# Performance work log

Measured on AMD Instinct MI355X. Metric: run time of the kernel, lower is better.

Reference implementation:

```python
import jax, jax.numpy as jnp
import numpy as np

N = 50000   # nodes
E = 600000  # edges
D = 128     # emb_dim
L = 5       # num_layers
ATOM_DIMS = np.array([119, 4, 11, 13, 11, 7, 13, 2, 9]) + 5   # per-feature vocab (+5 as in source)
BOND_DIMS = np.array([7, 22, 2]) + 5
BL_CENTERS = np.arange(0.0, 2.0, 0.1, dtype=np.float32)   # 20 centers, gamma 10
PR_CENTERS = np.arange(0.0, 1.0, 0.05, dtype=np.float32)  # 20 centers, gamma 1
BL_GAMMA = 10.0
PR_GAMMA = 1.0
BN_EPS = 1e-5


def setup_inputs() -> dict:
    key = jax.random.key(0)
    ks = jax.random.split(key, 16)
    scale = 1.0 / np.sqrt(D)
    atom_off = jnp.asarray(np.concatenate([[0], np.cumsum(ATOM_DIMS)[:-1]]), jnp.int32)
    bond_off = jnp.asarray(np.concatenate([[0], np.cumsum(BOND_DIMS)[:-1]]), jnp.int32)
    return {
        "x": jax.random.randint(ks[0], (N, 9), 0, 7, dtype=jnp.int32),
        "edge_index": jax.random.randint(ks[1], (2, E), 0, N, dtype=jnp.int32),
        "edge_attr_int": jax.random.randint(ks[2], (E, 3), 0, 7, dtype=jnp.int32),
        "edge_attr_float": jax.random.uniform(ks[3], (E, 2), dtype=jnp.float32),
        "atom_off": atom_off,
        "bond_off": bond_off,
        "atom_emb": jax.random.normal(ks[4], (int(ATOM_DIMS.sum()), D), jnp.float32) * scale,
        "bond_emb": jax.random.normal(ks[5], (L, int(BOND_DIMS.sum()), D), jnp.float32) * scale,
        "W_bl": jax.random.normal(ks[6], (L, len(BL_CENTERS), D), jnp.float32) * scale,
        "b_bl": jnp.zeros((L, D), jnp.float32),
        "W_pr": jax.random.normal(ks[7], (L, len(PR_CENTERS), D), jnp.float32) * scale,
        "b_pr": jnp.zeros((L, D), jnp.float32),
        "mlp_W1": jax.random.normal(ks[8], (L, D, D), jnp.float32) * scale,
        "mlp_b1": jnp.zeros((L, D), jnp.float32),
        "bn1_g": jnp.ones((L, D), jnp.float32),
        "bn1_b": jnp.zeros((L, D), jnp.float32),
        "mlp_W2": jax.random.normal(ks[9], (L, D, D), jnp.float32) * scale,
        "mlp_b2": jnp.zeros((L, D), jnp.float32),
        "eps_gin": jnp.zeros((L,), jnp.float32),
        "bn_g": jnp.ones((L, D), jnp.float32),
        "bn_b": jnp.zeros((L, D), jnp.float32),
    }


def _bn(h, g, b):
    # BatchNorm1d, training-mode batch statistics over the node axis
    m = h.mean(0)
    v = h.var(0)
    return (h - m) * jax.lax.rsqrt(v + BN_EPS) * g + b


def _rbf(x, centers, gamma):
    # exp(-gamma * (x - c)^2): [E] -> [E, n_centers]
    return jnp.exp(-gamma * jnp.square(x[:, None] - centers[None, :]))


def reference(x, edge_index, edge_attr_int, edge_attr_float, atom_off, bond_off,
              atom_emb, bond_emb, W_bl, b_bl, W_pr, b_pr,
              mlp_W1, mlp_b1, bn1_g, bn1_b, mlp_W2, mlp_b2,
              eps_gin, bn_g, bn_b):
    # AtomEncoder: sum of 9 categorical embeddings (flat table + offsets)
    h = atom_emb[x + atom_off[None, :]].sum(1)  # [N, D]
    src, dst = edge_index[0], edge_index[1]
    bl = _rbf(edge_attr_float[:, 0], jnp.asarray(BL_CENTERS), BL_GAMMA)  # [E, 20]
    pr = _rbf(edge_attr_float[:, 1], jnp.asarray(PR_CENTERS), PR_GAMMA)  # [E, 20]
    for l in range(L):
        # per-layer edge embedding: BondEncoder + BondFloatRBF
        e = bond_emb[l][edge_attr_int + bond_off[None, :]].sum(1)
        e = e + bl @ W_bl[l] + b_bl[l] + pr @ W_pr[l] + b_pr[l]
        # GINConv (aggr='add'): mlp((1+eps)*x + sum_j relu(x_j + e_ij))
        msg = jax.nn.relu(h[src] + e)                       # [E, D]
        agg = jax.ops.segment_sum(msg, dst, num_segments=N)  # [N, D]
        z = (1.0 + eps_gin[l]) * h + agg
        z = z @ mlp_W1[l] + mlp_b1[l]
        z = jax.nn.relu(_bn(z, bn1_g[l], bn1_b[l]))
        z = z @ mlp_W2[l] + mlp_b2[l]
        # outer per-layer BatchNorm; ReLU except last layer (drop_ratio=0)
        z = _bn(z, bn_g[l], bn_b[l])
        if l < L - 1:
            z = jax.nn.relu(z)
        h = z
    return h  # JK='last'
```

## Files before the change

kernel.cpp:

```cpp
#include <hip/hip_runtime.h>
#include <hip/hip_bf16.h>

#define GN 50000
#define GE 600000
#define DD 128
#define TQ 4096
#define NBOND 2268
#define TROWS (2*(TQ+1) + NBOND)
#define SCB 49
#define NBANK 16
#define SSET (NBANK*256)
#define NB 782
#define LDA2 132

typedef __attribute__((ext_vector_type(8))) short short8;
typedef __attribute__((ext_vector_type(4))) float floatx4;

__device__ __forceinline__ unsigned short f2b(float f) {
    __hip_bfloat16 h = __float2bfloat16(f);
    return __builtin_bit_cast(unsigned short, h);
}
__device__ __forceinline__ float b2f_lo(unsigned int u) { return __uint_as_float(u << 16); }
__device__ __forceinline__ float b2f_hi(unsigned int u) { return __uint_as_float(u & 0xffff0000u); }
__device__ __forceinline__ float bs2f(short s) {
    return __uint_as_float(((unsigned int)(unsigned short)s) << 16);
}

__global__ __launch_bounds__(256) void atom_kernel(
    const int* __restrict__ x, const int* __restrict__ atom_off,
    const float* __restrict__ atom_emb, unsigned short* __restrict__ h)
{
    int t = blockIdx.x * 256 + threadIdx.x;
    if (t >= GN * DD) return;
    int n = t >> 7, d = t & 127;
    float s = 0.f;
#pragma unroll
    for (int f = 0; f < 9; f++) {
        int idx = x[n * 9 + f] + atom_off[f];
        s += atom_emb[idx * DD + d];
    }
    h[t] = f2b(s);
}

__global__ __launch_bounds__(256) void hist_kernel(const int* __restrict__ ei, int* __restrict__ count)
{
    int e = blockIdx.x * 256 + threadIdx.x;
    if (e < GE) atomicAdd(&count[ei[GE + e]], 1);
}

__global__ __launch_bounds__(1024) void scan1_kernel(
    const int* __restrict__ count, int* __restrict__ row_start, int* __restrict__ blocksum)
{
    __shared__ int sh[1024];
    int t = threadIdx.x;
    int idx = blockIdx.x * 1024 + t;
    int v = (idx < GN) ? count[idx] : 0;
    sh[t] = v;
    __syncthreads();
    for (int off = 1; off < 1024; off <<= 1) {
        int u = (t >= off) ? sh[t - off] : 0;
        __syncthreads();
        sh[t] += u;
        __syncthreads();
    }
    if (idx <= GN) row_start[idx] = (t == 0) ? 0 : sh[t - 1];
    if (t == 1023) blocksum[blockIdx.x] = sh[1023];
}

__global__ __launch_bounds__(64) void scan2_kernel(
    const int* __restrict__ blocksum, int* __restrict__ blockoff)
{
    int t = threadIdx.x;
    int v = (t < SCB) ? blocksum[t] : 0;
#pragma unroll
    for (int off = 1; off < 64; off <<= 1) {
        int u = __shfl_up(v, off);
        if (t >= off) v += u;
    }
    int e = __shfl_up(v, 1);
    if (t == 0) e = 0;
    if (t < SCB) blockoff[t] = e;
}

__global__ __launch_bounds__(1024) void scan3_kernel(
    int* __restrict__ row_start, const int* __restrict__ blockoff)
{
    int idx = blockIdx.x * 1024 + threadIdx.x;
    if (idx <= GN) row_start[idx] += blockoff[blockIdx.x];
}

__global__ __launch_bounds__(256) void scatter_kernel(
    const int* __restrict__ ei, const int* __restrict__ eai, const float* __restrict__ eaf,
    const int* __restrict__ row_start, int* __restrict__ fill, int4* __restrict__ ep)
{
    int e = blockIdx.x * 256 + threadIdx.x;
    if (e < GE) {
        int d = ei[GE + e];
        int p = row_start[d] + atomicAdd(&fill[d], 1);
        int src = ei[e];
        float x1 = eaf[2 * e], x2 = eaf[2 * e + 1];
        int q1 = (int)(x1 * (float)TQ + 0.5f); q1 = min(max(q1, 0), TQ);
        int q2 = (int)(x2 * (float)TQ + 0.5f); q2 = min(max(q2, 0), TQ);
        int b0 = eai[3 * e], b1 = eai[3 * e + 1], b2 = eai[3 * e + 2];
        ep[p] = make_int4(src, q1 | (q2 << 16), (b0 * 27 + b1) * 7 + b2, 0);
    }
}

__global__ __launch_bounds__(128) void tables_kernel(
    const float* __restrict__ W_bl, const float* __restrict__ b_bl,
    const float* __restrict__ W_pr, const float* __restrict__ b_pr,
    const float* __restrict__ bond_emb, const int* __restrict__ bond_off,
    unsigned short* __restrict__ tbl_bl, unsigned short* __restrict__ tbl_pr,
    unsigned short* __restrict__ tbl_bond)
{
    int l = blockIdx.x / TROWS;
    int b = blockIdx.x % TROWS;
    int d = threadIdx.x;
    const float* W_bl_l = W_bl + (size_t)l * 20 * DD;
    const float* W_pr_l = W_pr + (size_t)l * 20 * DD;
    const float* bemb_l = bond_emb + (size_t)l * 46 * DD;
    if (b < (TQ + 1)) {
        float xq = b * (1.0f / TQ);
        float s = b_bl[(size_t)l * DD + d] + b_pr[(size_t)l * DD + d];
#pragma unroll
        for (int k = 0; k < 20; k++) {
            float dl = xq - 0.1f * k;
            s += __expf(-10.f * dl * dl) * W_bl_l[k * DD + d];
        }
        tbl_bl[((size_t)l * (TQ + 1) + b) * DD + d] = f2b(s);
    } else if (b < 2 * (TQ + 1)) {
        int q = b - (TQ + 1);
        float xq = q * (1.0f / TQ);
        float s = 0.f;
#pragma unroll
        for (int k = 0; k < 20; k++) {
            float dl = xq - 0.05f * k;
            s += __expf(-dl * dl) * W_pr_l[k * DD + d];
        }
        tbl_pr[((size_t)l * (TQ + 1) + q) * DD + d] = f2b(s);
    } else {
        int r = b - 2 * (TQ + 1);
        int b0 = r / 189;
        int rem = r % 189;
        int b1 = rem / 7, b2 = rem % 7;
        tbl_bond[((size_t)l * NBOND + r) * DD + d] =
            f2b(bemb_l[(b0 + bond_off[0]) * DD + d]
              + bemb_l[(b1 + bond_off[1]) * DD + d]
              + bemb_l[(b2 + bond_off[2]) * DD + d]);
    }
}

__global__ __launch_bounds__(256) void wfrag_kernel(
    const float* __restrict__ W1, const float* __restrict__ W2,
    unsigned short* __restrict__ wf_hi, unsigned short* __restrict__ wf_lo)
{
    int t = blockIdx.x * 256 + threadIdx.x;
    if (t >= 10 * 2048) return;
    int mat = t >> 11;
    int rem = t & 2047;
    int kt = rem >> 9;
    int rem2 = rem & 511;
    int nt = rem2 >> 6;
    int lane = rem2 & 63;
    const float* src = (mat & 1) ? (W2 + (size_t)(mat >> 1) * DD * DD)
                                 : (W1 + (size_t)(mat >> 1) * DD * DD);
    int n = nt * 16 + (lane & 15);
    int k0 = kt * 32 + (lane >> 4) * 8;
    size_t base = (size_t)mat * 16384 + (size_t)((kt * 8 + nt) * 64 + lane) * 8;
#pragma unroll
    for (int j = 0; j < 8; j++) {
        float w = src[(size_t)(k0 + j) * DD + n];
        unsigned short hi = f2b(w);
        wf_hi[base + j] = hi;
        wf_lo[base + j] = f2b(w - bs2f((short)hi));
    }
}

__global__ __launch_bounds__(256) void edge_kernel(
    const int4* __restrict__ ep,
    const unsigned short* __restrict__ tbl_bl, const unsigned short* __restrict__ tbl_pr,
    const unsigned short* __restrict__ tbl_bond,
    const unsigned short* __restrict__ hsrc, const int* __restrict__ row_start,
    const float* __restrict__ eps_gin, int layer, int apply_bn,
    const float* __restrict__ stats_prev, const float* __restrict__ g_prev,
    const float* __restrict__ b_prev,
    float* __restrict__ A)
{
    __shared__ float sc_s[DD], tr_s[DD];
    int tid = threadIdx.x;
    if (tid < DD) {
        float sc = 1.f, tr = 0.f;
        if (apply_bn) {
            float s = 0.f, q = 0.f;
#pragma unroll
            for (int bk = 0; bk < NBANK; bk++) {
                s += stats_prev[bk * 256 + tid];
                q += stats_prev[bk * 256 + 128 + tid];
            }
            float m = s * (1.0f / GN);
            float v = q * (1.0f / GN) - m * m;
            sc = g_prev[tid] * rsqrtf(v + 1e-5f);
            tr = b_prev[tid] - m * sc;
        }
        sc_s[tid] = sc;
        tr_s[tid] = tr;
    }
    __syncthreads();

    int wid = __builtin_amdgcn_readfirstlane(tid >> 6);
    int lane = tid & 63;
    float sc0 = sc_s[2 * lane],     tr0 = tr_s[2 * lane];
    float sc1 = sc_s[2 * lane + 1], tr1 = tr_s[2 * lane + 1];
    float rmin = apply_bn ? 0.f : -__builtin_inff();

    int n = blockIdx.x * 4 + wid;
    int s0 = __builtin_amdgcn_readfirstlane(row_start[n]);
    int s1 = __builtin_amdgcn_readfirstlane(row_start[n + 1]);
    const unsigned int* hu = (const unsigned int*)hsrc;
    const unsigned int* tb = (const unsigned int*)tbl_bl;
    const unsigned int* tp = (const unsigned int*)tbl_pr;
    const unsigned int* tg = (const unsigned int*)tbl_bond;
    float a0 = 0.f, a1 = 0.f;
    int p = s0;
    for (; p + 2 <= s1; p += 2) {
        int4 m0 = ep[p];
        int4 m1 = ep[p + 1];
        unsigned int ub0 = tb[(size_t)(m0.y & 0xffff) * 64 + lane];
        unsigned int up0 = tp[(size_t)((unsigned)m0.y >> 16) * 64 + lane];
        unsigned int ug0 = tg[(size_t)m0.z * 64 + lane];
        unsigned int uh0 = hu[(size_t)m0.x * 64 + lane];
        unsigned int ub1 = tb[(size_t)(m1.y & 0xffff) * 64 + lane];
        unsigned int up1 = tp[(size_t)((unsigned)m1.y >> 16) * 64 + lane];
        unsigned int ug1 = tg[(size_t)m1.z * 64 + lane];
        unsigned int uh1 = hu[(size_t)m1.x * 64 + lane];
        float h00 = fmaxf(fmaf(b2f_lo(uh0), sc0, tr0), rmin);
        float h01 = fmaxf(fmaf(b2f_hi(uh0), sc1, tr1), rmin);
        float h10 = fmaxf(fmaf(b2f_lo(uh1), sc0, tr0), rmin);
        float h11 = fmaxf(fmaf(b2f_hi(uh1), sc1, tr1), rmin);
        a0 += fmaxf(h00 + b2f_lo(ub0) + b2f_lo(up0) + b2f_lo(ug0), 0.f);
        a1 += fmaxf(h01 + b2f_hi(ub0) + b2f_hi(up0) + b2f_hi(ug0), 0.f);
        a0 += fmaxf(h10 + b2f_lo(ub1) + b2f_lo(up1) + b2f_lo(ug1), 0.f);
        a1 += fmaxf(h11 + b2f_hi(ub1) + b2f_hi(up1) + b2f_hi(ug1), 0.f);
    }
    if (p < s1) {
        int4 m0 = ep[p];
        unsigned int ub0 = tb[(size_t)(m0.y & 0xffff) * 64 + lane];
        unsigned int up0 = tp[(size_t)((unsigned)m0.y >> 16) * 64 + lane];
        unsigned int ug0 = tg[(size_t)m0.z * 64 + lane];
        unsigned int uh0 = hu[(size_t)m0.x * 64 + lane];
        float h00 = fmaxf(fmaf(b2f_lo(uh0), sc0, tr0), rmin);
        float h01 = fmaxf(fmaf(b2f_hi(uh0), sc1, tr1), rmin);
        a0 += fmaxf(h00 + b2f_lo(ub0) + b2f_lo(up0) + b2f_lo(ug0), 0.f);
        a1 += fmaxf(h01 + b2f_hi(ub0) + b2f_hi(up0) + b2f_hi(ug0), 0.f);
    }
    float eps1 = 1.f + eps_gin[layer];
    unsigned int un = hu[(size_t)n * 64 + lane];
    a0 += eps1 * fmaxf(fmaf(b2f_lo(un), sc0, tr0), rmin);
    a1 += eps1 * fmaxf(fmaf(b2f_hi(un), sc1, tr1), rmin);
    float2 o; o.x = a0; o.y = a1;
    *(float2*)(A + (size_t)n * DD + 2 * lane) = o;
}

template <int MODE>
__global__ __launch_bounds__(256) void gemm_kernel(
    const float* __restrict__ Asrc,
    const unsigned short* __restrict__ wf_hi, const unsigned short* __restrict__ wf_lo,
    const float* __restrict__ bias,
    unsigned short* __restrict__ Cbf, float* __restrict__ Cf32, int out_bf16,
    const float* __restrict__ stats_in, const float* __restrict__ bn_g,
    const float* __restrict__ bn_b, float* __restrict__ stats_out)
{
    __shared__ float At[64 * LDA2];
    __shared__ float sc_s[DD], tr_s[DD];
    int tid = threadIdx.x, wid = tid >> 6, lane = tid & 63;
    int row0 = blockIdx.x * 64;

    if (MODE == 1) {
        if (tid < DD) {
            float s = 0.f, q = 0.f;
#pragma unroll
            for (int bk = 0; bk < NBANK; bk++) {
                s += stats_in[bk * 256 + tid];
                q += stats_in[bk * 256 + 128 + tid];
            }
            float m = s * (1.0f / GN);
            float v = q * (1.0f / GN) - m * m;
            float sc = bn_g[tid] * rsqrtf(v + 1e-5f);
            sc_s[tid] = sc;
            tr_s[tid] = bn_b[tid] - m * sc;
        }
    }

    {
        const float* g = Asrc + (size_t)row0 * DD;
#pragma unroll
        for (int i = 0; i < 8; i++) {
            int idx = i * 1024 + tid * 4;
            float4 v = *(const float4*)(g + idx);
            int r = idx >> 7, c = idx & 127;
            *(float4*)(At + r * LDA2 + c) = v;
        }
    }
    __syncthreads();

    int quad = lane >> 4, l16 = lane & 15;
    floatx4 acc[4][2];
#pragma unroll
    for (int rt = 0; rt < 4; rt++)
#pragma unroll
        for (int nt = 0; nt < 2; nt++) acc[rt][nt] = (floatx4){0.f, 0.f, 0.f, 0.f};

    const short8* bhp = (const short8*)wf_hi;
    const short8* blp = (const short8*)wf_lo;
#pragma unroll
    for (int kt = 0; kt < 4; kt++) {
        short8 ahi[4], alo[4];
        int kb = kt * 32 + quad * 8;
#pragma unroll
        for (int rt = 0; rt < 4; rt++) {
            const float* ap = At + (rt * 16 + l16) * LDA2 + kb;
            float a[8];
            *(float4*)(a)     = *(const float4*)(ap);
            *(float4*)(a + 4) = *(const float4*)(ap + 4);
            if (MODE == 1) {
#pragma unroll
                for (int j = 0; j < 8; j++)
                    a[j] = fmaxf(a[j] * sc_s[kb + j] + tr_s[kb + j], 0.f);
            }
#pragma unroll
            for (int j = 0; j < 8; j++) {
                unsigned short hi = f2b(a[j]);
                ahi[rt][j] = (short)hi;
                alo[rt][j] = (short)f2b(a[j] - bs2f((short)hi));
            }
        }
#pragma unroll
        for (int nt = 0; nt < 2; nt++) {
            int ntg = wid * 2 + nt;
            short8 bhi = bhp[(kt * 8 + ntg) * 64 + lane];
            short8 blo = blp[(kt * 8 + ntg) * 64 + lane];
#pragma unroll
            for (int rt = 0; rt < 4; rt++) {
                acc[rt][nt] = __builtin_amdgcn_mfma_f32_16x16x32_bf16(ahi[rt], bhi, acc[rt][nt], 0, 0, 0);
                acc[rt][nt] = __builtin_amdgcn_mfma_f32_16x16x32_bf16(alo[rt], bhi, acc[rt][nt], 0, 0, 0);
                acc[rt][nt] = __builtin_amdgcn_mfma_f32_16x16x32_bf16(ahi[rt], blo, acc[rt][nt], 0, 0, 0);
            }
        }
    }

    int bank = blockIdx.x & (NBANK - 1);
#pragma unroll
    for (int nt = 0; nt < 2; nt++) {
        int col = (wid * 2 + nt) * 16 + l16;
        float bv = bias[col];
        float s = 0.f, q = 0.f;
#pragma unroll
        for (int rt = 0; rt < 4; rt++) {
#pragma unroll
            for (int v = 0; v < 4; v++) {
                int r = row0 + rt * 16 + quad * 4 + v;
                float o = acc[rt][nt][v] + bv;
                if (r < GN) {
                    s += o; q += o * o;
                    if (MODE == 1 && out_bf16) Cbf[(size_t)r * DD + col] = f2b(o);
                    else                       Cf32[(size_t)r * DD + col] = o;
                }
            }
        }
        s += __shfl_xor(s, 16); s += __shfl_xor(s, 32);
        q += __shfl_xor(q, 16); q += __shfl_xor(q, 32);
        if (lane < 16) {
            atomicAdd(&stats_out[bank * 256 + col], s);
            atomicAdd(&stats_out[bank * 256 + 128 + col], q);
        }
    }
}

__global__ __launch_bounds__(256) void bn_apply_kernel(
    const float* __restrict__ Z, const float* __restrict__ stats2,
    const float* __restrict__ g, const float* __restrict__ b,
    float* __restrict__ fout)
{
    __shared__ float sc_s[DD], tr_s[DD];
    int tid = threadIdx.x;
    if (tid < DD) {
        float s = 0.f, q = 0.f;
#pragma unroll
        for (int bk = 0; bk < NBANK; bk++) {
            s += stats2[bk * 256 + tid];
            q += stats2[bk * 256 + 128 + tid];
        }
        float m = s * (1.0f / GN);
        float v = q * (1.0f / GN) - m * m;
        float sc = g[tid] * rsqrtf(v + 1e-5f);
        sc_s[tid] = sc;
        tr_s[tid] = b[tid] - m * sc;
    }
    __syncthreads();
    const int total = GN * DD;
    for (int t = blockIdx.x * 256 + tid; t < total; t += gridDim.x * 256) {
        int c = t & 127;
        fout[t] = Z[t] * sc_s[c] + tr_s[c];
    }
}

extern "C" void kernel_launch(void* const* d_in, const int* in_sizes, int n_in,
                              void* d_out, int out_size, void* d_ws, size_t ws_size,
                              hipStream_t stream)
{
    const int*   x        = (const int*)d_in[0];
    const int*   ei       = (const int*)d_in[1];
    const int*   eai      = (const int*)d_in[2];
    const float* eaf      = (const float*)d_in[3];
    const int*   atom_off = (const int*)d_in[4];
    const int*   bond_off = (const int*)d_in[5];
    const float* atom_emb = (const float*)d_in[6];
    const float* bond_emb = (const float*)d_in[7];
    const float* W_bl     = (const float*)d_in[8];
    const float* b_bl     = (const float*)d_in[9];
    const float* W_pr     = (const float*)d_in[10];
    const float* b_pr     = (const float*)d_in[11];
    const float* W1       = (const float*)d_in[12];
    const float* b1       = (const float*)d_in[13];
    const float* bn1g     = (const float*)d_in[14];
    const float* bn1b     = (const float*)d_in[15];
    const float* W2       = (const float*)d_in[16];
    const float* b2       = (const float*)d_in[17];
    const float* eps_gin  = (const float*)d_in[18];
    const float* bng      = (const float*)d_in[19];
    const float* bnb      = (const float*)d_in[20];
    float* out = (float*)d_out;

    char* p = (char*)d_ws;
    unsigned short* h_bf  = (unsigned short*)p;  p += (size_t)GN * DD * 2;
    unsigned short* z2_bf = (unsigned short*)p;  p += (size_t)GN * DD * 2;
    float* A              = (float*)p;           p += (size_t)GN * DD * 4;
    float* z1             = (float*)p;           p += (size_t)GN * DD * 4;
    float* z2f            = (float*)p;           p += (size_t)GN * DD * 4;
    unsigned short* tbl_bl   = (unsigned short*)p;  p += (size_t)5 * (TQ + 1) * DD * 2;
    unsigned short* tbl_pr   = (unsigned short*)p;  p += (size_t)5 * (TQ + 1) * DD * 2;
    unsigned short* tbl_bond = (unsigned short*)p;  p += (size_t)5 * NBOND * DD * 2;
    unsigned short* wf_hi    = (unsigned short*)p;  p += (size_t)10 * 16384 * 2;
    unsigned short* wf_lo    = (unsigned short*)p;  p += (size_t)10 * 16384 * 2;
    float* stats_all = (float*)p;  p += (size_t)10 * SSET * 4;
    int* count    = (int*)p;    p += (size_t)GN * 4;
    int* fill     = (int*)p;    p += (size_t)GN * 4;
    int* row_start= (int*)p;    p += (size_t)(GN + 1) * 4;
    int* blocksum = (int*)p;    p += (size_t)SCB * 4;
    int* blockoff = (int*)p;    p += (size_t)SCB * 4;
    p = (char*)(((size_t)p + 15) & ~(size_t)15);
    int4* ep      = (int4*)p;   p += (size_t)GE * 16;

    hipMemsetAsync(count, 0, (size_t)GN * 4, stream);
    hipMemsetAsync(fill,  0, (size_t)GN * 4, stream);
    hipMemsetAsync(stats_all, 0, (size_t)10 * SSET * 4, stream);

    hist_kernel<<<(GE + 255) / 256, 256, 0, stream>>>(ei, count);
    scan1_kernel<<<SCB, 1024, 0, stream>>>(count, row_start, blocksum);
    scan2_kernel<<<1, 64, 0, stream>>>(blocksum, blockoff);
    scan3_kernel<<<SCB, 1024, 0, stream>>>(row_start, blockoff);
    scatter_kernel<<<(GE + 255) / 256, 256, 0, stream>>>(ei, eai, eaf, row_start, fill, ep);
    atom_kernel<<<(GN * DD + 255) / 256, 256, 0, stream>>>(x, atom_off, atom_emb, h_bf);
    wfrag_kernel<<<80, 256, 0, stream>>>(W1, W2, wf_hi, wf_lo);
    tables_kernel<<<5 * TROWS, 128, 0, stream>>>(
        W_bl, b_bl, W_pr, b_pr, bond_emb, bond_off, tbl_bl, tbl_pr, tbl_bond);

    for (int l = 0; l < 5; l++) {
        float* stats1 = stats_all + (size_t)(2 * l + 0) * SSET;
        float* stats2 = stats_all + (size_t)(2 * l + 1) * SSET;
        float* stats2_prev = stats_all + (size_t)(2 * (l - 1) + 1) * SSET;

        edge_kernel<<<GN / 4, 256, 0, stream>>>(
            ep,
            tbl_bl + (size_t)l * (TQ + 1) * DD,
            tbl_pr + (size_t)l * (TQ + 1) * DD,
            tbl_bond + (size_t)l * NBOND * DD,
            (l == 0) ? h_bf : z2_bf, row_start, eps_gin, l,
            (l > 0) ? 1 : 0,
            (l > 0) ? stats2_prev : stats_all,
            bng + (size_t)(l > 0 ? l - 1 : 0) * DD,
            bnb + (size_t)(l > 0 ? l - 1 : 0) * DD,
            A);

        gemm_kernel<0><<<NB, 256, 0, stream>>>(
            A, wf_hi + (size_t)(l * 2 + 0) * 16384, wf_lo + (size_t)(l * 2 + 0) * 16384,
            b1 + (size_t)l * DD, nullptr, z1, 0,
            nullptr, nullptr, nullptr, stats1);

        gemm_kernel<1><<<NB, 256, 0, stream>>>(
            z1, wf_hi + (size_t)(l * 2 + 1) * 16384, wf_lo + (size_t)(l * 2 + 1) * 16384,
            b2 + (size_t)l * DD, z2_bf, z2f, (l < 4) ? 1 : 0,
            stats1, bn1g + (size_t)l * DD, bn1b + (size_t)l * DD, stats2);
    }

    bn_apply_kernel<<<1024, 256, 0, stream>>>(
        z2f, stats_all + (size_t)9 * SSET, bng + (size_t)4 * DD, bnb + (size_t)4 * DD, out);
}
```

Before: 688.1 us.

## Switch edge aggregation to edge-parallel segmented atomics with separate BN prep pass

The per-destination-node edge kernel, where one wavefront walks a variable-length CSR row, is replaced by an edge-parallel kernel. Each wavefront takes 64 dst-sorted edges, accumulates runs that share a destination and flushes them with float atomics into A. A new hprep kernel applies the previous layer's BatchNorm and ReLU once per node, writes a bf16 copy of h, and initialises A with (1+eps)*h. Src and bond code are packed into one int so the dst can be stored, which assumes node index and bond code each fit in 16 bits. The change is meant to fix load imbalance and remove repeated BN math per edge, at the cost of an extra pass over the nodes, atomic traffic, and a now non-deterministic summation order.

```diff
diff --git a/kernel.cpp b/kernel.cpp
--- a/kernel.cpp
+++ b/kernel.cpp
@@ -12,6 +12,7 @@
 #define SSET (NBANK*256)
 #define NB 782
 #define LDA2 132
+#define EW (GE/64)
 
 typedef __attribute__((ext_vector_type(8))) short short8;
 typedef __attribute__((ext_vector_type(4))) float floatx4;
@@ -102,7 +103,8 @@
         int q1 = (int)(x1 * (float)TQ + 0.5f); q1 = min(max(q1, 0), TQ);
         int q2 = (int)(x2 * (float)TQ + 0.5f); q2 = min(max(q2, 0), TQ);
         int b0 = eai[3 * e], b1 = eai[3 * e + 1], b2 = eai[3 * e + 2];
-        ep[p] = make_int4(src, q1 | (q2 << 16), (b0 * 27 + b1) * 7 + b2, 0);
+        int bc = (b0 * 27 + b1) * 7 + b2;
+        ep[p] = make_int4(src | (bc << 16), q1 | (q2 << 16), d, 0);
     }
 }
 
@@ -176,89 +178,99 @@
     }
 }
 
+template <int L0>
+__global__ __launch_bounds__(256) void hprep_kernel(
+    const unsigned short* __restrict__ h_bf, const float* __restrict__ z2f,
+    const float* __restrict__ stats_prev, const float* __restrict__ g_prev,
+    const float* __restrict__ b_prev, const float* __restrict__ eps_gin, int layer,
+    unsigned short* __restrict__ hb, float* __restrict__ A)
+{
+    __shared__ float sc_s[DD], tr_s[DD];
+    int tid = threadIdx.x;
+    if (!L0) {
+        if (tid < DD) {
+            float s = 0.f, q = 0.f;
+#pragma unroll
+            for (int bk = 0; bk < NBANK; bk++) {
+                s += stats_prev[bk * 256 + tid];
+                q += stats_prev[bk * 256 + 128 + tid];
+            }
+            float m = s * (1.0f / GN);
+            float v = q * (1.0f / GN) - m * m;
+            float sc = g_prev[tid] * rsqrtf(v + 1e-5f);
+            sc_s[tid] = sc;
+            tr_s[tid] = b_prev[tid] - m * sc;
+        }
+        __syncthreads();
+    }
+    float eps1 = 1.f + eps_gin[layer];
+    const int total = GN * 64;
+    for (int t = blockIdx.x * 256 + tid; t < total; t += gridDim.x * 256) {
+        int d0 = (t & 63) * 2;
+        float f0, f1;
+        if (L0) {
+            unsigned int u = ((const unsigned int*)h_bf)[t];
+            f0 = b2f_lo(u); f1 = b2f_hi(u);
+        } else {
+            float2 z = ((const float2*)z2f)[t];
+            f0 = fmaxf(z.x * sc_s[d0] + tr_s[d0], 0.f);
+            f1 = fmaxf(z.y * sc_s[d0 + 1] + tr_s[d0 + 1], 0.f);
+            ((unsigned int*)hb)[t] = ((unsigned int)f2b(f1) << 16) | f2b(f0);
+        }
+        float2 o; o.x = eps1 * f0; o.y = eps1 * f1;
+        ((float2*)A)[t] = o;
+    }
+}
+
 __global__ __launch_bounds__(256) void edge_kernel(
     const int4* __restrict__ ep,
     const unsigned short* __restrict__ tbl_bl, const unsigned short* __restrict__ tbl_pr,
     const unsigned short* __restrict__ tbl_bond,
-    const unsigned short* __restrict__ hsrc, const int* __restrict__ row_start,
-    const float* __restrict__ eps_gin, int layer, int apply_bn,
-    const float* __restrict__ stats_prev, const float* __restrict__ g_prev,
-    const float* __restrict__ b_prev,
+    const unsigned short* __restrict__ hb,
     float* __restrict__ A)
 {
-    __shared__ float sc_s[DD], tr_s[DD];
     int tid = threadIdx.x;
-    if (tid < DD) {
-        float sc = 1.f, tr = 0.f;
-        if (apply_bn) {
-            float s = 0.f, q = 0.f;
-#pragma unroll
-            for (int bk = 0; bk < NBANK; bk++) {
-                s += stats_prev[bk * 256 + tid];
-                q += stats_prev[bk * 256 + 128 + tid];
-            }
-            float m = s * (1.0f / GN);
-            float v = q * (1.0f / GN) - m * m;
-            sc = g_prev[tid] * rsqrtf(v + 1e-5f);
-            tr = b_prev[tid] - m * sc;
-        }
-        sc_s[tid] = sc;
-        tr_s[tid] = tr;
-    }
-    __syncthreads();
-
-    int wid = __builtin_amdgcn_readfirstlane(tid >> 6);
+    int gw = blockIdx.x * 4 + (tid >> 6);
+    if (gw >= EW) return;
     int lane = tid & 63;
-    float sc0 = sc_s[2 * lane],     tr0 = tr_s[2 * lane];
-    float sc1 = sc_s[2 * lane + 1], tr1 = tr_s[2 * lane + 1];
-    float rmin = apply_bn ? 0.f : -__builtin_inff();
-
-    int n = blockIdx.x * 4 + wid;
-    int s0 = __builtin_amdgcn_readfirstlane(row_start[n]);
-    int s1 = __builtin_amdgcn_readfirstlane(row_start[n + 1]);
-    const unsigned int* hu = (const unsigned int*)hsrc;
+
+    int4 mv = ep[(size_t)gw * 64 + lane];
+
+    const unsigned int* hu = (const unsigned int*)hb;
     const unsigned int* tb = (const unsigned int*)tbl_bl;
     const unsigned int* tp = (const unsigned int*)tbl_pr;
     const unsigned int* tg = (const unsigned int*)tbl_bond;
+
     float a0 = 0.f, a1 = 0.f;
-    int p = s0;
-    for (; p + 2 <= s1; p += 2) {
-        int4 m0 = ep[p];
-        int4 m1 = ep[p + 1];
-        unsigned int ub0 = tb[(size_t)(m0.y & 0xffff) * 64 + lane];
-        unsigned int up0 = tp[(size_t)((unsigned)m0.y >> 16) * 64 + lane];
-        unsigned int ug0 = tg[(size_t)m0.z * 64 + lane];
-        unsigned int uh0 = hu[(size_t)m0.x * 64 + lane];
-        unsigned int ub1 = tb[(size_t)(m1.y & 0xffff) * 64 + lane];
-        unsigned int up1 = tp[(size_t)((unsigned)m1.y >> 16) * 64 + lane];
-        unsigned int ug1 = tg[(size_t)m1.z * 64 + lane];
-        unsigned int uh1 = hu[(size_t)m1.x * 64 + lane];
-        float h00 = fmaxf(fmaf(b2f_lo(uh0), sc0, tr0), rmin);
-        float h01 = fmaxf(fmaf(b2f_hi(uh0), sc1, tr1), rmin);
-        float h10 = fmaxf(fmaf(b2f_lo(uh1), sc0, tr0), rmin);
-        float h11 = fmaxf(fmaf(b2f_hi(uh1), sc1, tr1), rmin);
-        a0 += fmaxf(h00 + b2f_lo(ub0) + b2f_lo(up0) + b2f_lo(ug0), 0.f);
-        a1 += fmaxf(h01 + b2f_hi(ub0) + b2f_hi(up0) + b2f_hi(ug0), 0.f);
-        a0 += fmaxf(h10 + b2f_lo(ub1) + b2f_lo(up1) + b2f_lo(ug1), 0.f);
-        a1 += fmaxf(h11 + b2f_hi(ub1) + b2f_hi(up1) + b2f_hi(ug1), 0.f);
-    }
-    if (p < s1) {
-        int4 m0 = ep[p];
-        unsigned int ub0 = tb[(size_t)(m0.y & 0xffff) * 64 + lane];
-        unsigned int up0 = tp[(size_t)((unsigned)m0.y >> 16) * 64 + lane];
-        unsigned int ug0 = tg[(size_t)m0.z * 64 + lane];
-        unsigned int uh0 = hu[(size_t)m0.x * 64 + lane];
-        float h00 = fmaxf(fmaf(b2f_lo(uh0), sc0, tr0), rmin);
-        float h01 = fmaxf(fmaf(b2f_hi(uh0), sc1, tr1), rmin);
-        a0 += fmaxf(h00 + b2f_lo(ub0) + b2f_lo(up0) + b2f_lo(ug0), 0.f);
-        a1 += fmaxf(h01 + b2f_hi(ub0) + b2f_hi(up0) + b2f_hi(ug0), 0.f);
-    }
-    float eps1 = 1.f + eps_gin[layer];
-    unsigned int un = hu[(size_t)n * 64 + lane];
-    a0 += eps1 * fmaxf(fmaf(b2f_lo(un), sc0, tr0), rmin);
-    a1 += eps1 * fmaxf(fmaf(b2f_hi(un), sc1, tr1), rmin);
-    float2 o; o.x = a0; o.y = a1;
-    *(float2*)(A + (size_t)n * DD + 2 * lane) = o;
+    int cur = __builtin_amdgcn_readlane(mv.z, 0);
+
+    for (int b = 0; b < 8; b++) {
+        unsigned int ub[8], up[8], ug[8], uh[8];
+#pragma unroll
+        for (int u = 0; u < 8; u++) {
+            int j = b * 8 + u;
+            unsigned int sx = (unsigned int)__builtin_amdgcn_readlane(mv.x, j);
+            unsigned int q  = (unsigned int)__builtin_amdgcn_readlane(mv.y, j);
+            ub[u] = tb[(size_t)(q & 0xffff) * 64 + lane];
+            up[u] = tp[(size_t)(q >> 16) * 64 + lane];
+            ug[u] = tg[(size_t)(sx >> 16) * 64 + lane];
+            uh[u] = hu[(size_t)(sx & 0xffff) * 64 + lane];
+        }
+#pragma unroll
+        for (int u = 0; u < 8; u++) {
+            int j = b * 8 + u;
+            int dstj = __builtin_amdgcn_readlane(mv.z, j);
+            if (dstj != cur) {
+                unsafeAtomicAdd(&A[(size_t)cur * DD + 2 * lane],     a0);
+                unsafeAtomicAdd(&A[(size_t)cur * DD + 2 * lane + 1], a1);
+                a0 = 0.f; a1 = 0.f; cur = dstj;
+            }
+            a0 += fmaxf(b2f_lo(uh[u]) + b2f_lo(ub[u]) + b2f_lo(up[u]) + b2f_lo(ug[u]), 0.f);
+            a1 += fmaxf(b2f_hi(uh[u]) + b2f_hi(ub[u]) + b2f_hi(up[u]) + b2f_hi(ug[u]), 0.f);
+        }
+    }
+    unsafeAtomicAdd(&A[(size_t)cur * DD + 2 * lane],     a0);
+    unsafeAtomicAdd(&A[(size_t)cur * DD + 2 * lane + 1], a1);
 }
 
 template <int MODE>
@@ -266,7 +278,7 @@
     const float* __restrict__ Asrc,
     const unsigned short* __restrict__ wf_hi, const unsigned short* __restrict__ wf_lo,
     const float* __restrict__ bias,
-    unsigned short* __restrict__ Cbf, float* __restrict__ Cf32, int out_bf16,
+    float* __restrict__ Cf32,
     const float* __restrict__ stats_in, const float* __restrict__ bn_g,
     const float* __restrict__ bn_b, float* __restrict__ stats_out)
 {
@@ -362,8 +374,7 @@
                 float o = acc[rt][nt][v] + bv;
                 if (r < GN) {
                     s += o; q += o * o;
-                    if (MODE == 1 && out_bf16) Cbf[(size_t)r * DD + col] = f2b(o);
-                    else                       Cf32[(size_t)r * DD + col] = o;
+                    Cf32[(size_t)r * DD + col] = o;
                 }
             }
         }
@@ -433,7 +444,7 @@
 
     char* p = (char*)d_ws;
     unsigned short* h_bf  = (unsigned short*)p;  p += (size_t)GN * DD * 2;
-    unsigned short* z2_bf = (unsigned short*)p;  p += (size_t)GN * DD * 2;
+    unsigned short* hb    = (unsigned short*)p;  p += (size_t)GN * DD * 2;
     float* A              = (float*)p;           p += (size_t)GN * DD * 4;
     float* z1             = (float*)p;           p += (size_t)GN * DD * 4;
     float* z2f            = (float*)p;           p += (size_t)GN * DD * 4;
@@ -470,26 +481,32 @@
         float* stats2 = stats_all + (size_t)(2 * l + 1) * SSET;
         float* stats2_prev = stats_all + (size_t)(2 * (l - 1) + 1) * SSET;
 
-        edge_kernel<<<GN / 4, 256, 0, stream>>>(
+        if (l == 0) {
+            hprep_kernel<1><<<1024, 256, 0, stream>>>(
+                h_bf, nullptr, nullptr, nullptr, nullptr, eps_gin, l, nullptr, A);
+        } else {
+            hprep_kernel<0><<<1024, 256, 0, stream>>>(
+                nullptr, z2f, stats2_prev,
+                bng + (size_t)(l - 1) * DD, bnb + (size_t)(l - 1) * DD,
+                eps_gin, l, hb, A);
+        }
+
+        edge_kernel<<<(EW + 3) / 4, 256, 0, stream>>>(
             ep,
             tbl_bl + (size_t)l * (TQ + 1) * DD,
             tbl_pr + (size_t)l * (TQ + 1) * DD,
             tbl_bond + (size_t)l * NBOND * DD,
-            (l == 0) ? h_bf : z2_bf, row_start, eps_gin, l,
-            (l > 0) ? 1 : 0,
-            (l > 0) ? stats2_prev : stats_all,
-            bng + (size_t)(l > 0 ? l - 1 : 0) * DD,
-            bnb + (size_t)(l > 0 ? l - 1 : 0) * DD,
+            (l == 0) ? h_bf : hb,
             A);
 
         gemm_kernel<0><<<NB, 256, 0, stream>>>(
             A, wf_hi + (size_t)(l * 2 + 0) * 16384, wf_lo + (size_t)(l * 2 + 0) * 16384,
-            b1 + (size_t)l * DD, nullptr, z1, 0,
+            b1 + (size_t)l * DD, z1,
             nullptr, nullptr, nullptr, stats1);
 
         gemm_kernel<1><<<NB, 256, 0, stream>>>(
             z1, wf_hi + (size_t)(l * 2 + 1) * 16384, wf_lo + (size_t)(l * 2 + 1) * 16384,
-            b2 + (size_t)l * DD, z2_bf, z2f, (l < 4) ? 1 : 0,
+            b2 + (size_t)l * DD, z2f,
             stats1, bn1g + (size_t)l * DD, bn1b + (size_t)l * DD, stats2);
     }
 
```

New measurement: 801.0 us. 16.4% more time.
